# Kernel tuning notes

Hardware: AMD Instinct MI355X
Metric: run time of the kernel (lower is better)

The kernel has to match this reference:

```python
import jax, jax.numpy as jnp
import numpy as np

B, T, DIM = 1, 2048, 1024
NUM_HEADS, HEAD_DIM = 8, 128
ATTN_SCALE = 0.12


def _rms_norm(x):
    # F.rms_norm(x, x.size(-1)) with no weight; eps defaults to machine eps
    eps = jnp.asarray(jnp.finfo(x.dtype).eps, x.dtype)
    return x * jax.lax.rsqrt(jnp.mean(x * x, axis=-1, keepdims=True) + eps)


def _rotary_tables(seq_len, head_dim):
    # (1/1024) ** linspace(0,1,head_dim//4), then pad with head_dim//4 zeros
    freq = (1.0 / 1024.0) ** jnp.linspace(0.0, 1.0, head_dim // 4, dtype=jnp.float32)
    ang = jnp.concatenate([freq, jnp.zeros(head_dim // 4, jnp.float32)])  # [hd/2]
    theta = jnp.arange(seq_len, dtype=jnp.float32)[:, None] * ang[None, :]  # [T, hd/2]
    return jnp.cos(theta), jnp.sin(theta)


def _apply_rotary(x, cos, sin):
    # x: [B, T, H, hd]
    x1, x2 = jnp.split(x.astype(jnp.float32), 2, axis=-1)
    c = cos[None, :, None, :]
    s = sin[None, :, None, :]
    y1 = x1 * c + x2 * s
    y2 = -x1 * s + x2 * c
    return jnp.concatenate([y1, y2], axis=-1).astype(x.dtype)


def setup_inputs() -> dict:
    key = jax.random.key(0)
    ks = jax.random.split(key, 5)
    bound = (3.0 ** 0.5) * 0.5 * DIM ** (-0.5)
    x = jax.random.normal(ks[0], (B, T, DIM), jnp.float32)
    ve = jax.random.normal(ks[1], (B, T, NUM_HEADS * HEAD_DIM), jnp.float32)
    qkv_w = jax.random.uniform(ks[2], (3, NUM_HEADS * HEAD_DIM, DIM), jnp.float32, -bound, bound)
    lambdas = jnp.array([0.5, 0.5], jnp.float32)
    # original zero-inits c_proj; use small random weight so the output is nontrivial
    c_proj_w = jax.random.uniform(ks[3], (DIM, NUM_HEADS * HEAD_DIM), jnp.float32, -bound, bound)
    return {"x": x, "ve": ve, "qkv_w": qkv_w, "lambdas": lambdas, "c_proj_w": c_proj_w}


def reference(x, ve, qkv_w, lambdas, c_proj_w):
    Bx, Tx, D = x.shape
    H, hd = NUM_HEADS, HEAD_DIM
    # fused QKV projection: weight [3*H*hd, D]
    qkv = x @ qkv_w.reshape(3 * H * hd, D).T            # [B, T, 3*H*hd]
    qkv = qkv.reshape(Bx, Tx, 3 * H, hd)
    q, k, v = jnp.split(qkv, 3, axis=-2)                # each [B, T, H, hd]
    q, k = _rms_norm(q), _rms_norm(k)
    cos, sin = _rotary_tables(Tx, hd)
    q, k = _apply_rotary(q, cos, sin), _apply_rotary(k, cos, sin)
    v = lambdas[0] * v + lambdas[1] * ve.reshape(v.shape)
    att = jnp.einsum('bthd,bshd->bhts', q, k) * ATTN_SCALE
    causal = jnp.tril(jnp.ones((Tx, Tx), bool))
    att = jnp.where(causal[None, None], att, -jnp.inf)
    att = jax.nn.softmax(att, axis=-1)
    y = jnp.einsum('bhts,bshd->bthd', att, v).reshape(Bx, Tx, H * hd)
    return y @ c_proj_w.T
```

## Files before the change

kernel.cpp:

```cpp
#include <hip/hip_runtime.h>


typedef __attribute__((ext_vector_type(8))) short short8;
typedef __attribute__((ext_vector_type(4))) short short4b;
typedef __attribute__((ext_vector_type(4))) float fx4;
typedef __attribute__((ext_vector_type(8))) unsigned short ushort8;
typedef __attribute__((ext_vector_type(4))) unsigned short ushort4v;
typedef __attribute__((ext_vector_type(2))) unsigned short ushort2v;
typedef __attribute__((ext_vector_type(4))) float float4v;

#define T_SEQ 2048
#define NH 8
#define HD 128

__device__ __forceinline__ unsigned short f2bf(float f) {
  union { float f; unsigned u; } v; v.f = f;
  unsigned u = v.u;
  u += 0x7fffu + ((u >> 16) & 1u);
  return (unsigned short)(u >> 16);
}
__device__ __forceinline__ short bf_t(float f) {
  union { float f; unsigned u; } v; v.f = f;
  return (short)(v.u >> 16);
}
__device__ __forceinline__ float bf2f(unsigned short h) {
  union { unsigned u; float f; } v; v.u = ((unsigned)h) << 16;
  return v.f;
}

typedef __attribute__((address_space(1))) unsigned int glb_u32;
typedef __attribute__((address_space(3))) unsigned int lds_u32;
__device__ __forceinline__ void gl_lds16(const unsigned short* g, unsigned short* l) {
  __builtin_amdgcn_global_load_lds((const glb_u32*)g, (lds_u32*)l, 16, 0, 0);
}

__global__ __launch_bounds__(256) void cast3_kernel(
    const float* __restrict__ x, const float* __restrict__ w1,
    const float* __restrict__ w2, unsigned short* __restrict__ o) {
  long q = (long)blockIdx.x * 256 + threadIdx.x;
  const float* src;
  if (q < 524288)        src = x  + 4 * q;
  else if (q < 1310720)  src = w1 + 4 * (q - 524288);
  else                   src = w2 + 4 * (q - 1310720);
  float4v v = *(const float4v*)src;
  ushort4v r;
  r[0] = f2bf(v[0]); r[1] = f2bf(v[1]); r[2] = f2bf(v[2]); r[3] = f2bf(v[3]);
  *(ushort4v*)(o + 4 * q) = r;
}

template <bool OUT_BF16, int BM, int BN>
__global__ __launch_bounds__(256) void gemm_bt4(
    const unsigned short* __restrict__ A, const unsigned short* __restrict__ B,
    void* __restrict__ Cp, int M, int N, int K) {
  constexpr int MT = BM / 32;
  constexpr int NT = BN / 32;
  constexpr int ASEG = BM / 8;
  constexpr int NLOAD = (BM + BN) / 32;
  __shared__ unsigned short a_sh[2][BM * 64];
  __shared__ unsigned short b_sh[2][BN * 64];
  const int tid = threadIdx.x;
  const int wave = tid >> 6, lane = tid & 63;
  const int ln = lane & 15, quad = lane >> 4;
  const int wm = wave & 1, wn = wave >> 1;
  const long arow0 = (long)blockIdx.y * BM;
  const long brow0 = (long)blockIdx.x * BN;

  const unsigned short* gsrc[NLOAD];
  unsigned short* ldst[NLOAD];
  int bstr[NLOAD];
  for (int i = 0; i < NLOAD; ++i) {
    int s = wave * NLOAD + i;
    int isB = s >= ASEG;
    int srel = isB ? s - ASEG : s;
    int li = srel * 64 + lane;
    int row = li >> 3, posc = li & 7;
    int c = posc ^ (row & 7);
    gsrc[i] = (isB ? B + brow0 * (long)K : A + arow0 * (long)K)
              + (long)row * K + c * 8;
    ldst[i] = (isB ? &b_sh[0][0] : &a_sh[0][0]) + srel * 512;
    bstr[i] = isB ? BN * 64 : BM * 64;
  }
  for (int i = 0; i < NLOAD; ++i) gl_lds16(gsrc[i], ldst[i]);

  fx4 acc[MT][NT] = {};
  int cur = 0;
  for (int k0 = 0; k0 < K; k0 += 64, cur ^= 1) {
    __syncthreads();
    if (k0 + 64 < K)
      for (int i = 0; i < NLOAD; ++i)
        gl_lds16(gsrc[i] + k0 + 64, ldst[i] + (cur ^ 1) * bstr[i]);
    const unsigned short* ash = &a_sh[cur][0];
    const unsigned short* bsh = &b_sh[cur][0];
    short8 af[2][MT], bfr[2][NT];
    for (int kq = 0; kq < 2; ++kq) {
      for (int mt = 0; mt < MT; ++mt) {
        int m = wm * (BM / 2) + mt * 16 + ln;
        int pos = (kq * 4 + quad) ^ (m & 7);
        af[kq][mt] = *(const short8*)&ash[m * 64 + pos * 8];
      }
      for (int nt = 0; nt < NT; ++nt) {
        int n = wn * (BN / 2) + nt * 16 + ln;
        int pos = (kq * 4 + quad) ^ (n & 7);
        bfr[kq][nt] = *(const short8*)&bsh[n * 64 + pos * 8];
      }
    }
    for (int kq = 0; kq < 2; ++kq)
      for (int mt = 0; mt < MT; ++mt)
        for (int nt = 0; nt < NT; ++nt)
          acc[mt][nt] = __builtin_amdgcn_mfma_f32_16x16x32_bf16(
              af[kq][mt], bfr[kq][nt], acc[mt][nt], 0, 0, 0);
  }
  for (int mt = 0; mt < MT; ++mt)
    for (int nt = 0; nt < NT; ++nt)
      for (int r = 0; r < 4; ++r) {
        long row = arow0 + wm * (BM / 2) + mt * 16 + quad * 4 + r;
        long col = brow0 + wn * (BN / 2) + nt * 16 + ln;
        float v = acc[mt][nt][r];
        if constexpr (OUT_BF16)
          ((unsigned short*)Cp)[row * N + col] = f2bf(v);
        else
          ((float*)Cp)[row * N + col] = v;
      }
}

__global__ __launch_bounds__(256) void prep_qkv(
    const unsigned short* __restrict__ qkv, const float* __restrict__ ve,
    const float* __restrict__ lambdas, unsigned short* __restrict__ qh,
    unsigned short* __restrict__ kh, unsigned short* __restrict__ vt) {
  __shared__ unsigned short lt[64 * 72];
  const int bx = blockIdx.x, h = blockIdx.y;
  const int tid = threadIdx.x;

  if (bx < 128) {
    const int r2 = tid >> 5, c = tid & 31;
    float ang[2];
    for (int u = 0; u < 2; ++u) {
      int dd = 2 * c + u;
      ang[u] = (dd < 32) ? exp2f(-10.0f * (float)dd / 31.0f) : 0.0f;
    }
    for (int rr = 0; rr < 2; ++rr) {
      int t = bx * 16 + rr * 8 + r2;
      float cv[2], sv[2];
      for (int u = 0; u < 2; ++u) {
        float th = (float)t * ang[u];
        sv[u] = __sinf(th); cv[u] = __cosf(th);
      }
      for (int which = 0; which < 2; ++which) {
        const unsigned short* src = qkv + (long)t * 3072 + which * 1024 + h * 128;
        ushort2v aa = *(const ushort2v*)(src + 2 * c);
        ushort2v bb = *(const ushort2v*)(src + 64 + 2 * c);
        float x1[2] = { bf2f(aa[0]), bf2f(aa[1]) };
        float x2[2] = { bf2f(bb[0]), bf2f(bb[1]) };
        float ss = x1[0]*x1[0] + x1[1]*x1[1] + x2[0]*x2[0] + x2[1]*x2[1];
        for (int off = 1; off < 32; off <<= 1) ss += __shfl_xor(ss, off);
        float rn = rsqrtf(ss * (1.0f / 128.0f) + 1.1920929e-7f);
        ushort2v o1, o2;
        for (int u = 0; u < 2; ++u) {
          float y1 = ( x1[u] * cv[u] + x2[u] * sv[u]) * rn;
          float y2 = (-x1[u] * sv[u] + x2[u] * cv[u]) * rn;
          o1[u] = f2bf(y1); o2[u] = f2bf(y2);
        }
        unsigned short* dst = (which ? kh : qh) + ((long)h * T_SEQ + t) * 128;
        *(ushort2v*)(dst + 2 * c) = o1;
        *(ushort2v*)(dst + 64 + 2 * c) = o2;
      }
    }
  } else {
    const int vb = bx - 128;
    const int tt = vb >> 1, dsub = vb & 1;
    const float l0 = lambdas[0], l1 = lambdas[1];
    const int r = tid >> 2, cb = (tid & 3) * 16;
    const unsigned short* vs = qkv + (long)(tt * 64 + r) * 3072 + 2048
                               + h * 128 + dsub * 64 + cb;
    const float* es = ve + (long)(tt * 64 + r) * 1024 + h * 128 + dsub * 64 + cb;
    ushort8 vv[2];
    for (int q = 0; q < 2; ++q) vv[q] = *(const ushort8*)(vs + 8 * q);
    float4v ee[4];
    for (int q = 0; q < 4; ++q) ee[q] = *(const float4v*)(es + 4 * q);
    for (int j = 0; j < 16; ++j) {
      float v = bf2f(vv[j >> 3][j & 7]) * l0 + ee[j >> 2][j & 3] * l1;
      lt[(cb + j) * 72 + r] = f2bf(v);
    }
    __syncthreads();
    const int d = tid >> 2, quarter = tid & 3;
    unsigned short* dst = vt + ((long)h * HD + dsub * 64 + d) * T_SEQ
                          + tt * 64 + quarter * 16;
    const unsigned short* srcl = &lt[d * 72];
    for (int g = 0; g < 4; ++g) {
      int p0 = quarter * 16 + g * 4;
      int kv0 = ((p0 >> 5) & 1) * 32 + ((p0 >> 2) & 1) * 16 + ((p0 >> 3) & 3) * 4;
      *(ushort4v*)(dst + g * 4) = *(const ushort4v*)(srcl + kv0);
    }
  }
}

#define ATT_C1 0.17312340490667562f
#define ATT_C2 23.083120654223415f

__global__ __launch_bounds__(256, 2) void attn_part(
    const unsigned short* __restrict__ qh, const unsigned short* __restrict__ kh,
    const unsigned short* __restrict__ vt, unsigned short* __restrict__ Yp,
    float* __restrict__ lp) {
  __shared__ unsigned short kbuf[2][8192];
  __shared__ unsigned short vbuf[2][8192];
  const int tid = threadIdx.x;
  const int wave = tid >> 6, lane = tid & 63;
  const int ln = lane & 15, quad = lane >> 4;
  const int qt = blockIdx.x, h = blockIdx.y, ch = blockIdx.z;
  const int jmax = 2 * qt + 1;
  const int j0 = ch * 4;
  if (j0 > jmax) return;
  const int j1 = min(j0 + 3, jmax);

  int qg[2];
  short8 qf[2][4];
  for (int s = 0; s < 2; ++s) {
    qg[s] = qt * 128 + wave * 32 + s * 16 + ln;
    const unsigned short* qbase = qh + ((long)h * T_SEQ + qg[s]) * 128;
    for (int kc = 0; kc < 4; ++kc)
      qf[s][kc] = *(const short8*)(qbase + kc * 32 + quad * 8);
  }
  fx4 accy[2][8] = {};
  float l_loc[2] = {0.f, 0.f};

  const unsigned short* kg[4]; unsigned short* kl[4];
  const unsigned short* vg[4]; unsigned short* vl[4];
  for (int i = 0; i < 4; ++i) {
    int s = wave * 4 + i;
    { int li = s * 64 + lane; int row = li >> 4, posc = li & 15;
      int c = posc ^ (row & 15);
      kg[i] = kh + ((long)h * T_SEQ + row) * 128 + c * 8;
      kl[i] = &kbuf[0][s * 512]; }
    { int li = s * 64 + lane; int row = li >> 3, posc = li & 7;
      int c = posc ^ (row & 7);
      vg[i] = vt + ((long)h * HD + row) * T_SEQ + c * 8;
      vl[i] = &vbuf[0][s * 512]; }
  }
  for (int i = 0; i < 4; ++i) gl_lds16(kg[i] + (long)j0 * 8192, kl[i]);
  for (int i = 0; i < 4; ++i) gl_lds16(vg[i] + (long)j0 * 64, vl[i]);

  int cur = 0;
  for (int jt = j0; jt <= j1; ++jt, cur ^= 1) {
    __syncthreads();
    if (jt < j1) {
      int nb = (cur ^ 1) * 8192;
      for (int i = 0; i < 4; ++i) gl_lds16(kg[i] + (long)(jt + 1) * 8192, kl[i] + nb);
      for (int i = 0; i < 4; ++i) gl_lds16(vg[i] + (long)(jt + 1) * 64, vl[i] + nb);
    }
    const unsigned short* kb_ = &kbuf[cur][0];
    fx4 s4[2][4];
    for (int kt = 0; kt < 4; ++kt) {
      s4[0][kt] = fx4{0.f, 0.f, 0.f, 0.f};
      s4[1][kt] = fx4{0.f, 0.f, 0.f, 0.f};
      for (int kc = 0; kc < 4; ++kc) {
        int pos = (kc * 4 + quad) ^ ln;
        short8 kf = *(const short8*)&kb_[(kt * 16 + ln) * 128 + pos * 8];
        s4[0][kt] = __builtin_amdgcn_mfma_f32_16x16x32_bf16(kf, qf[0][kc], s4[0][kt], 0, 0, 0);
        s4[1][kt] = __builtin_amdgcn_mfma_f32_16x16x32_bf16(kf, qf[1][kc], s4[1][kt], 0, 0, 0);
      }
    }
    short4b pb[2][4];
    for (int s = 0; s < 2; ++s)
      for (int kt = 0; kt < 4; ++kt) {
        int kvb = jt * 64 + kt * 16 + quad * 4;
        float p[4];
        for (int r = 0; r < 4; ++r)
          p[r] = exp2f(fmaf(s4[s][kt][r], ATT_C1, -ATT_C2));
        if (jt * 64 + kt * 16 + 15 > qt * 128 + wave * 32 + s * 16) {
          for (int r = 0; r < 4; ++r) if (kvb + r > qg[s]) p[r] = 0.f;
        }
        l_loc[s] += (p[0] + p[1]) + (p[2] + p[3]);
        pb[s][kt] = short4b{ bf_t(p[0]), bf_t(p[1]), bf_t(p[2]), bf_t(p[3]) };
      }
    const unsigned short* vb_ = &vbuf[cur][0];
    for (int kh2 = 0; kh2 < 2; ++kh2) {
      for (int dt = 0; dt < 8; ++dt) {
        int row = dt * 16 + ln;
        int pos = (kh2 * 4 + quad) ^ (ln & 7);
        short8 va = *(const short8*)&vb_[row * 64 + pos * 8];
        short4b va0 = { va[0], va[1], va[2], va[3] };
        short4b va1 = { va[4], va[5], va[6], va[7] };
        for (int s = 0; s < 2; ++s) {
          accy[s][dt] = __builtin_amdgcn_mfma_f32_16x16x16bf16_1k(
              va0, pb[s][kh2 * 2], accy[s][dt], 0, 0, 0);
          accy[s][dt] = __builtin_amdgcn_mfma_f32_16x16x16bf16_1k(
              va1, pb[s][kh2 * 2 + 1], accy[s][dt], 0, 0, 0);
        }
      }
    }
  }

  int cbase = qt + ((qt - 1) * (qt - 1)) / 4;
  const long pp = (long)(h * 72 + cbase + ch);
  for (int s = 0; s < 2; ++s) {
    float l = l_loc[s];
    l += __shfl_xor(l, 16);
    l += __shfl_xor(l, 32);
    int q = wave * 32 + s * 16 + ln;
    if (quad == 0) lp[pp * 128 + q] = l;
    unsigned short* yb = Yp + pp * 16384 + (long)q * 128;
    for (int dt = 0; dt < 8; ++dt) {
      ushort4v o;
      for (int r = 0; r < 4; ++r) o[r] = f2bf(accy[s][dt][r]);
      *(ushort4v*)(yb + dt * 16 + quad * 4) = o;
    }
  }
}

__global__ __launch_bounds__(256) void attn_combine(
    const unsigned short* __restrict__ Yp, const float* __restrict__ lp,
    unsigned short* __restrict__ y) {
  const int bx = blockIdx.x, h = blockIdx.y;
  const int qt = bx >> 1, sub = bx & 1;
  const int tid = threadIdx.x;
  const int row = sub * 64 + (tid >> 2), cb = (tid & 3) * 32;
  const int nc = (qt >> 1) + 1;
  const int cbase = qt + ((qt - 1) * (qt - 1)) / 4;
  float acc[32];
  for (int j = 0; j < 32; ++j) acc[j] = 0.f;
  float ltot = 0.f;
  for (int c = 0; c < nc; ++c) {
    long pp = (long)(h * 72 + cbase + c);
    const unsigned short* ys = Yp + pp * 16384 + (long)row * 128 + cb;
    ltot += lp[pp * 128 + row];
    for (int q8 = 0; q8 < 4; ++q8) {
      ushort8 v = *(const ushort8*)(ys + q8 * 8);
      for (int j = 0; j < 8; ++j) acc[q8 * 8 + j] += bf2f(v[j]);
    }
  }
  float inv = 1.f / ltot;
  unsigned short* dst = y + (long)(qt * 128 + row) * 1024 + h * 128 + cb;
  for (int q8 = 0; q8 < 4; ++q8) {
    ushort8 o;
    for (int j = 0; j < 8; ++j) o[j] = f2bf(acc[q8 * 8 + j] * inv);
    *(ushort8*)(dst + q8 * 8) = o;
  }
}

extern "C" void kernel_launch(void* const* d_in, const int* in_sizes, int n_in,
                              void* d_out, int out_size, void* d_ws, size_t ws_size,
                              hipStream_t stream) {
  const float* x       = (const float*)d_in[0];
  const float* ve      = (const float*)d_in[1];
  const float* qkv_w   = (const float*)d_in[2];
  const float* lambdas = (const float*)d_in[3];
  const float* c_proj  = (const float*)d_in[4];
  char* ws = (char*)d_ws;
  unsigned short* qkv_bf = (unsigned short*)(ws);
  unsigned short* x_bf   = (unsigned short*)(ws + 12582912);
  unsigned short* wqkv   = (unsigned short*)(ws + 16777216);
  unsigned short* wproj  = (unsigned short*)(ws + 23068672);
  unsigned short* qhat   = (unsigned short*)(ws + 25165824);
  unsigned short* khat   = (unsigned short*)(ws + 29360128);
  unsigned short* vtb    = (unsigned short*)(ws + 33554432);
  unsigned short* ybf    = (unsigned short*)(ws + 37748736);
  unsigned short* Yp     = (unsigned short*)(ws);
  float*          lpart  = (float*)(ws + 18874368);
  float* out = (float*)d_out;

  cast3_kernel<<<6144, 256, 0, stream>>>(x, qkv_w, c_proj, x_bf);
  gemm_bt4<true, 64, 128><<<dim3(24, 32), 256, 0, stream>>>(x_bf, wqkv, qkv_bf, 2048, 3072, 1024);
  prep_qkv<<<dim3(192, 8), 256, 0, stream>>>(qkv_bf, ve, lambdas, qhat, khat, vtb);
  attn_part<<<dim3(16, 8, 8), 256, 0, stream>>>(qhat, khat, vtb, Yp, lpart);
  attn_combine<<<dim3(32, 8), 256, 0, stream>>>(Yp, lpart, ybf);
  gemm_bt4<false, 64, 64><<<dim3(16, 32), 256, 0, stream>>>(ybf, wproj, out, 2048, 1024, 1024);
}
```

Baseline: 173.2 us.

## Fuse attention combine into split-KV kernel via last-block atomic counter

Removes the separate attn_combine launch. Each split-KV attention block now increments an atomic per-(head, q-tile) counter, and the last-arriving block reduces the partial outputs into the bf16 y buffer. Query tiles are scheduled in reverse order so the heaviest tiles start first, the counters are zeroed inside prep_qkv, and GEMM occupancy hints and the output projection tile size are changed. It trades one launch and its tail for threadfence/atomic overhead and serialized combine work in the last block.

```diff
diff --git a/kernel.cpp b/kernel.cpp
--- a/kernel.cpp
+++ b/kernel.cpp
@@ -48,8 +48,8 @@
   *(ushort4v*)(o + 4 * q) = r;
 }
 
-template <bool OUT_BF16, int BM, int BN>
-__global__ __launch_bounds__(256) void gemm_bt4(
+template <bool OUT_BF16, int BM, int BN, int MINW>
+__global__ __launch_bounds__(256, MINW) void gemm_bt4(
     const unsigned short* __restrict__ A, const unsigned short* __restrict__ B,
     void* __restrict__ Cp, int M, int N, int K) {
   constexpr int MT = BM / 32;
@@ -126,10 +126,12 @@
 __global__ __launch_bounds__(256) void prep_qkv(
     const unsigned short* __restrict__ qkv, const float* __restrict__ ve,
     const float* __restrict__ lambdas, unsigned short* __restrict__ qh,
-    unsigned short* __restrict__ kh, unsigned short* __restrict__ vt) {
+    unsigned short* __restrict__ kh, unsigned short* __restrict__ vt,
+    int* __restrict__ cnt) {
   __shared__ unsigned short lt[64 * 72];
   const int bx = blockIdx.x, h = blockIdx.y;
   const int tid = threadIdx.x;
+  if (bx == 0 && h == 0 && tid < 128) cnt[tid] = 0;
 
   if (bx < 128) {
     const int r2 = tid >> 5, c = tid & 31;
@@ -200,13 +202,15 @@
 __global__ __launch_bounds__(256, 2) void attn_part(
     const unsigned short* __restrict__ qh, const unsigned short* __restrict__ kh,
     const unsigned short* __restrict__ vt, unsigned short* __restrict__ Yp,
-    float* __restrict__ lp) {
+    float* __restrict__ lp, unsigned short* __restrict__ ybf,
+    int* __restrict__ cnt) {
   __shared__ unsigned short kbuf[2][8192];
   __shared__ unsigned short vbuf[2][8192];
+  __shared__ int last_flag;
   const int tid = threadIdx.x;
   const int wave = tid >> 6, lane = tid & 63;
   const int ln = lane & 15, quad = lane >> 4;
-  const int qt = blockIdx.x, h = blockIdx.y, ch = blockIdx.z;
+  const int qt = 15 - (int)blockIdx.x, h = blockIdx.y, ch = blockIdx.z;
   const int jmax = 2 * qt + 1;
   const int j0 = ch * 4;
   if (j0 > jmax) return;
@@ -290,7 +294,7 @@
     }
   }
 
-  int cbase = qt + ((qt - 1) * (qt - 1)) / 4;
+  const int cbase = qt + ((qt - 1) * (qt - 1)) / 4;
   const long pp = (long)(h * 72 + cbase + ch);
   for (int s = 0; s < 2; ++s) {
     float l = l_loc[s];
@@ -305,35 +309,40 @@
       *(ushort4v*)(yb + dt * 16 + quad * 4) = o;
     }
   }
-}
-
-__global__ __launch_bounds__(256) void attn_combine(
-    const unsigned short* __restrict__ Yp, const float* __restrict__ lp,
-    unsigned short* __restrict__ y) {
-  const int bx = blockIdx.x, h = blockIdx.y;
-  const int qt = bx >> 1, sub = bx & 1;
-  const int tid = threadIdx.x;
-  const int row = sub * 64 + (tid >> 2), cb = (tid & 3) * 32;
+
   const int nc = (qt >> 1) + 1;
-  const int cbase = qt + ((qt - 1) * (qt - 1)) / 4;
-  float acc[32];
-  for (int j = 0; j < 32; ++j) acc[j] = 0.f;
-  float ltot = 0.f;
-  for (int c = 0; c < nc; ++c) {
-    long pp = (long)(h * 72 + cbase + c);
-    const unsigned short* ys = Yp + pp * 16384 + (long)row * 128 + cb;
-    ltot += lp[pp * 128 + row];
+  __threadfence();
+  __syncthreads();
+  if (tid == 0) {
+    int prev = atomicAdd(&cnt[h * 16 + qt], 1);
+    last_flag = (prev == nc - 1);
+  }
+  __syncthreads();
+  if (!last_flag) return;
+  __threadfence();
+
+  for (int sub = 0; sub < 2; ++sub) {
+    const int row = sub * 64 + (tid >> 2);
+    const int cb = (tid & 3) * 32;
+    float acc[32];
+    for (int j = 0; j < 32; ++j) acc[j] = 0.f;
+    float ltot = 0.f;
+    for (int c = 0; c < nc; ++c) {
+      long pc = (long)(h * 72 + cbase + c);
+      const unsigned short* ys = Yp + pc * 16384 + (long)row * 128 + cb;
+      ltot += lp[pc * 128 + row];
+      for (int q8 = 0; q8 < 4; ++q8) {
+        ushort8 v = *(const ushort8*)(ys + q8 * 8);
+        for (int j = 0; j < 8; ++j) acc[q8 * 8 + j] += bf2f(v[j]);
+      }
+    }
+    float inv = 1.f / ltot;
+    unsigned short* dst = ybf + (long)(qt * 128 + row) * 1024 + h * 128 + cb;
     for (int q8 = 0; q8 < 4; ++q8) {
-      ushort8 v = *(const ushort8*)(ys + q8 * 8);
-      for (int j = 0; j < 8; ++j) acc[q8 * 8 + j] += bf2f(v[j]);
-    }
-  }
-  float inv = 1.f / ltot;
-  unsigned short* dst = y + (long)(qt * 128 + row) * 1024 + h * 128 + cb;
-  for (int q8 = 0; q8 < 4; ++q8) {
-    ushort8 o;
-    for (int j = 0; j < 8; ++j) o[j] = f2bf(acc[q8 * 8 + j] * inv);
-    *(ushort8*)(dst + q8 * 8) = o;
+      ushort8 o;
+      for (int j = 0; j < 8; ++j) o[j] = f2bf(acc[q8 * 8 + j] * inv);
+      *(ushort8*)(dst + q8 * 8) = o;
+    }
   }
 }
 
@@ -356,12 +365,12 @@
   unsigned short* ybf    = (unsigned short*)(ws + 37748736);
   unsigned short* Yp     = (unsigned short*)(ws);
   float*          lpart  = (float*)(ws + 18874368);
+  int*            cnt    = (int*)(ws + 19169280);
   float* out = (float*)d_out;
 
   cast3_kernel<<<6144, 256, 0, stream>>>(x, qkv_w, c_proj, x_bf);
-  gemm_bt4<true, 64, 128><<<dim3(24, 32), 256, 0, stream>>>(x_bf, wqkv, qkv_bf, 2048, 3072, 1024);
-  prep_qkv<<<dim3(192, 8), 256, 0, stream>>>(qkv_bf, ve, lambdas, qhat, khat, vtb);
-  attn_part<<<dim3(16, 8, 8), 256, 0, stream>>>(qhat, khat, vtb, Yp, lpart);
-  attn_combine<<<dim3(32, 8), 256, 0, stream>>>(Yp, lpart, ybf);
-  gemm_bt4<false, 64, 64><<<dim3(16, 32), 256, 0, stream>>>(ybf, wproj, out, 2048, 1024, 1024);
-}
+  gemm_bt4<true, 64, 128, 3><<<dim3(24, 32), 256, 0, stream>>>(x_bf, wqkv, qkv_bf, 2048, 3072, 1024);
+  prep_qkv<<<dim3(192, 8), 256, 0, stream>>>(qkv_bf, ve, lambdas, qhat, khat, vtb, cnt);
+  attn_part<<<dim3(16, 8, 8), 256, 0, stream>>>(qhat, khat, vtb, Yp, lpart, ybf, cnt);
+  gemm_bt4<false, 32, 64, 4><<<dim3(16, 64), 256, 0, stream>>>(ybf, wproj, out, 2048, 1024, 1024);
+}
```

Measured after the change: 273.3 us. 57.8% more time.
